# Performance work log

Measured on AMD Instinct MI355X. Metric: run time of the kernel, lower is better.

## Reference

```python
import jax, jax.numpy as jnp
import numpy as np

TOP_K = 2  # matches init top_k


def setup_inputs() -> dict:
    key = jax.random.key(0)
    k = jax.random.split(key, 5)
    B, S, D, E, H = 8, 2048, 768, 8, 3072  # batch, seq, n_embed, num_experts, 4*n_embed
    init = lambda kk, shape: (jax.random.normal(kk, shape, jnp.float32) * 0.02)
    return {
        "x": jax.random.normal(k[0], (B, S, D), jnp.float32),
        "Wg": init(k[1], (D, E)),            # router weight
        "bg": jnp.zeros((E,), jnp.float32),   # router bias
        "W1": init(k[2], (E, D, H)),          # stacked expert fc1
        "b1": jnp.zeros((E, H), jnp.float32),
        "W2": init(k[3], (E, H, D)),          # stacked expert fc2
        "b2": jnp.zeros((E, D), jnp.float32),
    }


def _moe(x, Wg, bg, W1, b1, W2, b2):
    B, S, D = x.shape
    E = Wg.shape[1]
    # --- TopkRouter: top-k logits, softmax over selected experts, scatter to full gate tensor ---
    logits = x @ Wg + bg                                  # [B,S,E]
    top_vals, top_idx = jax.lax.top_k(logits, TOP_K)      # [B,S,K]
    gates_k = jax.nn.softmax(top_vals, axis=-1)           # softmax over the k selected experts only
    one_hot = jax.nn.one_hot(top_idx, E, dtype=x.dtype)   # [B,S,K,E] (E is small)
    gates = jnp.sum(one_hot * gates_k[..., None], axis=-2)  # [B,S,E], zeros off top-k

    # --- dispatch/compute/combine: scan over experts (fixed, small), gate-weighted accumulate ---
    flat_x = x.reshape(-1, D)          # [T,D]
    flat_g = gates.reshape(-1, E).T    # [E,T]

    def body(acc, p):
        W1e, b1e, W2e, b2e, ge = p
        h = jax.nn.relu(flat_x @ W1e + b1e)               # [T,H]
        acc = acc + (h @ W2e + b2e) * ge[:, None]         # gate==0 -> zero contribution (incl. bias)
        return acc, None

    out, _ = jax.lax.scan(body, jnp.zeros_like(flat_x), (W1, b1, W2, b2, flat_g))
    return out.reshape(B, S, D)


def reference(x, Wg, bg, W1, b1, W2, b2):
    return _moe(x, Wg, bg, W1, b1, W2, b2)
```

## Files before the change

kernel.cpp:

```cpp
#include <hip/hip_runtime.h>
#include <stdint.h>

typedef unsigned short u16;
typedef __attribute__((ext_vector_type(8))) short v8s;
typedef __attribute__((ext_vector_type(4))) float v4f;

#define T_TOK 16384
#define DIM   768
#define NE    8
#define HH    3072
#define CH    1536
#define MCAP  34816
#define GM    (MCAP/256)

#define O_W2T 0u
#define O_W1T 37748736u
#define O_XBF 75497472u
#define O_OB1 37748736u
#define O_STK 100663296u
#define O_SGT 100802560u
#define O_TE  100941824u
#define O_TG  101072896u
#define O_TS  101203968u
#define O_MET 101335040u
#define O_HBF 101335296u
#define O_OB0 208290048u
#define WS_TIER_A 261767424ull

__device__ __forceinline__ u16 f2bf(float f){
  uint32_t u = __float_as_uint(f);
  uint32_t r = (u + 0x7fffu + ((u >> 16) & 1u)) >> 16;
  return (u16)r;
}
__device__ __forceinline__ float bf2f(u16 v){
  return __uint_as_float(((uint32_t)v) << 16);
}
__device__ __forceinline__ void gll16(const u16* g, u16* l){
  __builtin_amdgcn_global_load_lds((const __attribute__((address_space(1))) uint32_t*)g,
                                   (__attribute__((address_space(3))) uint32_t*)l, 16, 0, 0);
}

#define BAR() do { asm volatile("" ::: "memory"); __builtin_amdgcn_s_barrier(); asm volatile("" ::: "memory"); } while(0)
#define WAIT_LGKM0() asm volatile("s_waitcnt lgkmcnt(0)" ::: "memory")
#define WAIT_VM4() asm volatile("s_waitcnt vmcnt(4)" ::: "memory")
#define WAIT_VM0() asm volatile("s_waitcnt vmcnt(0)" ::: "memory")

__global__ __launch_bounds__(256) void k_transpose(
    const float* __restrict__ src, u16* __restrict__ dst, int R, int C){
  __shared__ float tile[64][65];
  int e = blockIdx.z;
  int c0 = blockIdx.x * 64, r0 = blockIdx.y * 64;
  const float* s = src + (size_t)e * R * C;
  u16* d = dst + (size_t)e * R * C;
  int tx = threadIdx.x, ty = threadIdx.y;
  #pragma unroll
  for (int j = 0; j < 4; j++){
    float4 v = *(const float4*)&s[(size_t)(r0 + ty + 16*j) * C + c0 + tx*4];
    tile[ty+16*j][tx*4+0] = v.x; tile[ty+16*j][tx*4+1] = v.y;
    tile[ty+16*j][tx*4+2] = v.z; tile[ty+16*j][tx*4+3] = v.w;
  }
  __syncthreads();
  #pragma unroll
  for (int j = 0; j < 4; j++){
    int cc = ty + 16*j;
    ushort4 o;
    o.x = f2bf(tile[tx*4+0][cc]);
    o.y = f2bf(tile[tx*4+1][cc]);
    o.z = f2bf(tile[tx*4+2][cc]);
    o.w = f2bf(tile[tx*4+3][cc]);
    *(ushort4*)&d[(size_t)(c0 + cc) * R + r0 + tx*4] = o;
  }
}

__global__ __launch_bounds__(256) void k_router(
    const float* __restrict__ x, const float* __restrict__ Wg, const float* __restrict__ bg,
    int* __restrict__ tE, float* __restrict__ tG, u16* __restrict__ Xbf){
  int t = blockIdx.x * 4 + (threadIdx.x >> 6);
  int l = threadIdx.x & 63;
  const float4* xr4 = (const float4*)(x + (size_t)t * DIM);
  ushort4* xb4 = (ushort4*)(Xbf + (size_t)t * DIM);
  float acc[NE];
  #pragma unroll
  for (int e = 0; e < NE; e++) acc[e] = 0.f;
  #pragma unroll
  for (int j = 0; j < DIM / 256; j++){
    int c4 = l + 64 * j;
    float4 xv = xr4[c4];
    ushort4 o; o.x = f2bf(xv.x); o.y = f2bf(xv.y); o.z = f2bf(xv.z); o.w = f2bf(xv.w);
    xb4[c4] = o;
    float xs[4] = {xv.x, xv.y, xv.z, xv.w};
    #pragma unroll
    for (int q = 0; q < 4; q++){
      const float4* wr4 = (const float4*)(Wg + (size_t)(4*c4 + q) * NE);
      float4 w0 = wr4[0], w1 = wr4[1];
      acc[0] += xs[q]*w0.x; acc[1] += xs[q]*w0.y; acc[2] += xs[q]*w0.z; acc[3] += xs[q]*w0.w;
      acc[4] += xs[q]*w1.x; acc[5] += xs[q]*w1.y; acc[6] += xs[q]*w1.z; acc[7] += xs[q]*w1.w;
    }
  }
  #pragma unroll
  for (int off = 32; off; off >>= 1)
    #pragma unroll
    for (int e = 0; e < NE; e++) acc[e] += __shfl_xor(acc[e], off, 64);

  if (l == 0){
    float lgt[NE];
    #pragma unroll
    for (int e = 0; e < NE; e++) lgt[e] = acc[e] + bg[e];
    int i0 = 0; float v0 = lgt[0];
    #pragma unroll
    for (int e = 1; e < NE; e++) if (lgt[e] > v0){ v0 = lgt[e]; i0 = e; }
    int i1 = -1; float v1 = -1e30f;
    #pragma unroll
    for (int e = 0; e < NE; e++) if (e != i0 && lgt[e] > v1){ v1 = lgt[e]; i1 = e; }
    float ed = expf(v1 - v0);
    float g1 = ed / (1.f + ed);
    float g0 = 1.f / (1.f + ed);
    tE[2*t] = i0; tE[2*t+1] = i1;
    tG[2*t] = g0; tG[2*t+1] = g1;
  }
}

__global__ __launch_bounds__(256) void k_count(const int* __restrict__ tE, int* __restrict__ counts){
  int i = blockIdx.x * blockDim.x + threadIdx.x;
  int c[NE];
  #pragma unroll
  for (int e = 0; e < NE; e++) c[e] = 0;
  for (int j = i; j < 2 * T_TOK; j += 32 * 256){
    int v = tE[j];
    #pragma unroll
    for (int e = 0; e < NE; e++) c[e] += (v == e);
  }
  #pragma unroll
  for (int off = 32; off; off >>= 1)
    #pragma unroll
    for (int e = 0; e < NE; e++) c[e] += __shfl_xor(c[e], off, 64);
  if ((threadIdx.x & 63) == 0){
    #pragma unroll
    for (int e = 0; e < NE; e++) atomicAdd(&counts[e], c[e]);
  }
}

__global__ void k_scan(const int* __restrict__ counts, int* __restrict__ offs){
  if (threadIdx.x == 0){
    int o = 0;
    for (int e = 0; e < NE; e++){ offs[e] = o; o += (counts[e] + 255) & ~255; }
    offs[NE] = o;
  }
}

__global__ __launch_bounds__(256) void k_scatter(
    const int* __restrict__ tE, const float* __restrict__ tG,
    const int* __restrict__ offs, int* __restrict__ fill,
    int* __restrict__ slot_token, float* __restrict__ slot_gate, int* __restrict__ tSlot){
  int t = blockIdx.x * 256 + threadIdx.x;
  int lane = threadIdx.x & 63, w = threadIdx.x >> 6;
  int e0 = tE[2*t], e1 = tE[2*t+1];
  float g0 = tG[2*t], g1 = tG[2*t+1];

  __shared__ int wcnt[4][NE];
  __shared__ int woff[4][NE];
  __shared__ int bbase[NE];

  uint64_t below = (1ull << lane) - 1ull;
  int rank0 = 0, rank1 = 0;
  #pragma unroll
  for (int e = 0; e < NE; e++){
    uint64_t m0 = __ballot(e0 == e);
    uint64_t m1 = __ballot(e1 == e);
    int c0 = __popcll(m0);
    if (e0 == e) rank0 = __popcll(m0 & below);
    if (e1 == e) rank1 = c0 + __popcll(m1 & below);
    if (lane == 0) wcnt[w][e] = c0 + __popcll(m1);
  }
  __syncthreads();
  if (threadIdx.x < NE){
    int e = threadIdx.x;
    int s = 0;
    #pragma unroll
    for (int ww = 0; ww < 4; ww++){ woff[ww][e] = s; s += wcnt[ww][e]; }
    bbase[e] = atomicAdd(&fill[e], s);
  }
  __syncthreads();
  int p0 = offs[e0] + bbase[e0] + woff[w][e0] + rank0;
  slot_token[p0] = t; slot_gate[p0] = g0; tSlot[2*t] = p0;
  int p1 = offs[e1] + bbase[e1] + woff[w][e1] + rank1;
  slot_token[p1] = t; slot_gate[p1] = g1; tSlot[2*t+1] = p1;
}

__global__ void k_outinit(const int* __restrict__ tE, const float* __restrict__ tG,
                          const float* __restrict__ b2, float* __restrict__ out){
  int t = blockIdx.x;
  int e0 = tE[2*t], e1 = tE[2*t+1];
  float g0 = tG[2*t], g1 = tG[2*t+1];
  const float* r0 = b2 + (size_t)e0 * DIM;
  const float* r1 = b2 + (size_t)e1 * DIM;
  float* o = out + (size_t)t * DIM;
  #pragma unroll
  for (int j = 0; j < DIM / 256; j++){
    int c = threadIdx.x + 256 * j;
    o[c] = g0 * r0[c] + g1 * r1[c];
  }
}

#define ABASE(b,h) (((b)*2+(h))*8192)
#define BBASE(b,h) (32768 + ((b)*2+(h))*8192)
#define SWZE(ro,ks) (((((ro)*128) + (ks)*64 + lg*16) ^ (((lm)&7)<<4)) >> 1)

#define STAGE2(p0, p1, base, kk) do { \
  gll16((p0) + (kk), &lds[(base) + (w*2)*512]); \
  gll16((p1) + (kk), &lds[(base) + (w*2+1)*512]); } while(0)

#define MFMA_Q(MOFF, NOFF, BF) \
  __builtin_amdgcn_s_setprio(1); \
  _Pragma("unroll") \
  for (int mi = 0; mi < 4; mi++) \
    _Pragma("unroll") \
    for (int ni = 0; ni < 2; ni++) \
      _Pragma("unroll") \
      for (int ks = 0; ks < 2; ks++) \
        acc[(MOFF)+mi][(NOFF)+ni] = __builtin_amdgcn_mfma_f32_16x16x32_bf16(aF[mi][ks], BF[ni][ks], acc[(MOFF)+mi][(NOFF)+ni], 0, 0, 0); \
  __builtin_amdgcn_s_setprio(0);

__device__ __forceinline__ int find_expert(const int* offs, int grb, int& total){
  int offr[NE+1];
  #pragma unroll
  for (int i = 0; i <= NE; i++) offr[i] = offs[i];
  total = offr[NE];
  int e = 0;
  #pragma unroll
  for (int i = 1; i < NE; i++) e += (grb >= offr[i]);
  return e;
}

__global__ __launch_bounds__(512, 2) void k_gemm1(
    const u16* __restrict__ Xbf, const u16* __restrict__ W1t, const float* __restrict__ b1,
    const int* __restrict__ slot_token, const float* __restrict__ slot_gate,
    const int* __restrict__ offs, u16* __restrict__ Hbuf, int hs, int cbase, int ntc)
{
  int bid = blockIdx.x;
  int swz = (bid & 7) * ((int)gridDim.x >> 3) + (bid >> 3);
  int mt = swz / ntc, ntile = swz % ntc;
  int grb = mt * 256;
  int total;
  int e = find_expert(offs, grb, total);
  if (grb >= total) return;
  int nb = ntile * 256;
  int habs = cbase + nb;

  __shared__ __align__(16) u16 lds[65536];

  int tid = threadIdx.x, w = tid >> 6, lane = tid & 63;
  int wm = w >> 2, wn = w & 3, lm = lane & 15, lg = lane >> 4;
  int cbe = (((lane & 7) ^ (lane >> 3)) << 3);

  int rA00 = (w*2+0)*8 + (lane>>3), rA01 = (w*2+1)*8 + (lane>>3);
  const u16 *sA00 = Xbf + (size_t)slot_token[grb + rA00]       * DIM + cbe;
  const u16 *sA01 = Xbf + (size_t)slot_token[grb + rA01]       * DIM + cbe;
  const u16 *sA10 = Xbf + (size_t)slot_token[grb + 128 + rA00] * DIM + cbe;
  const u16 *sA11 = Xbf + (size_t)slot_token[grb + 128 + rA01] * DIM + cbe;
  const u16 *sB00 = W1t + ((size_t)e*HH + habs + rA00)       * DIM + cbe;
  const u16 *sB01 = W1t + ((size_t)e*HH + habs + rA01)       * DIM + cbe;
  const u16 *sB10 = W1t + ((size_t)e*HH + habs + 128 + rA00) * DIM + cbe;
  const u16 *sB11 = W1t + ((size_t)e*HH + habs + 128 + rA01) * DIM + cbe;

  v4f acc[8][4];
  #pragma unroll
  for (int mi = 0; mi < 8; mi++)
    #pragma unroll
    for (int ni = 0; ni < 4; ni++) acc[mi][ni] = 0.f;

  const int NTK = DIM / 64;
  STAGE2(sA00, sA01, ABASE(0,0), 0);  STAGE2(sA10, sA11, ABASE(0,1), 0);
  STAGE2(sB00, sB01, BBASE(0,0), 0);  STAGE2(sB10, sB11, BBASE(0,1), 0);
  STAGE2(sA00, sA01, ABASE(1,0), 64); STAGE2(sA10, sA11, ABASE(1,1), 64);
  WAIT_VM4(); BAR();

  v8s aF[4][2], bF0[2][2], bF1[2][2];
  for (int k = 0; k < NTK; ++k){
    int cur = k & 1, nx = cur ^ 1;
    int ab = ABASE(cur, wm);
    int bb = BBASE(cur, wn >> 1);
    #pragma unroll
    for (int mi = 0; mi < 4; mi++)
      #pragma unroll
      for (int ks = 0; ks < 2; ks++)
        aF[mi][ks] = *(const v8s*)&lds[ab + SWZE(mi*16 + lm, ks)];
    #pragma unroll
    for (int ni = 0; ni < 2; ni++)
      #pragma unroll
      for (int ks = 0; ks < 2; ks++)
        bF0[ni][ks] = *(const v8s*)&lds[bb + SWZE((wn&1)*64 + ni*16 + lm, ks)];
    if (k + 1 < NTK) STAGE2(sB00, sB01, BBASE(nx,0), (k+1)*64);
    MFMA_Q(0, 0, bF0);
    BAR();
    #pragma unroll
    for (int ni = 0; ni < 2; ni++)
      #pragma unroll
      for (int ks = 0; ks < 2; ks++)
        bF1[ni][ks] = *(const v8s*)&lds[bb + SWZE((wn&1)*64 + (2+ni)*16 + lm, ks)];
    if (k + 1 < NTK) STAGE2(sB10, sB11, BBASE(nx,1), (k+1)*64);
    MFMA_Q(0, 2, bF1);
    BAR();
    #pragma unroll
    for (int mi = 0; mi < 4; mi++)
      #pragma unroll
      for (int ks = 0; ks < 2; ks++)
        aF[mi][ks] = *(const v8s*)&lds[ab + SWZE((4+mi)*16 + lm, ks)];
    MFMA_Q(4, 0, bF0);
    WAIT_LGKM0(); BAR();
    if (k + 2 < NTK){
      STAGE2(sA00, sA01, ABASE(cur,0), (k+2)*64);
      STAGE2(sA10, sA11, ABASE(cur,1), (k+2)*64);
    }
    MFMA_Q(4, 2, bF1);
    if (k + 2 < NTK) { WAIT_VM4(); } else { WAIT_VM0(); }
    BAR();
  }

  float b1v[4];
  #pragma unroll
  for (int ni = 0; ni < 4; ni++) b1v[ni] = b1[(size_t)e * HH + habs + wn*64 + ni*16 + lm];
  #pragma unroll
  for (int mi = 0; mi < 8; mi++){
    int rbase = grb + wm*128 + mi*16 + lg*4;
    float g[4];
    #pragma unroll
    for (int i = 0; i < 4; i++) g[i] = slot_gate[rbase + i];
    #pragma unroll
    for (int ni = 0; ni < 4; ni++){
      int col = nb + wn*64 + ni*16 + lm;
      #pragma unroll
      for (int i = 0; i < 4; i++){
        float v = acc[mi][ni][i] + b1v[ni];
        v = fmaxf(v, 0.f) * g[i];
        Hbuf[(size_t)(rbase + i) * hs + col] = f2bf(v);
      }
    }
  }
}

__global__ __launch_bounds__(512, 2) void k_gemm2(
    const u16* __restrict__ Hbuf, const u16* __restrict__ W2t,
    const int* __restrict__ slot_token, const int* __restrict__ offs,
    float* __restrict__ out, u16* __restrict__ Obuf, int hs, int cbase, int klen, int mode)
{
  const int NT = DIM / 256;
  int bid = blockIdx.x;
  int swz = (bid & 7) * ((int)gridDim.x >> 3) + (bid >> 3);
  int mt = swz / NT, ntile = swz % NT;
  int grb = mt * 256;
  int total;
  int e = find_expert(offs, grb, total);
  if (grb >= total) return;
  int nb = ntile * 256;

  __shared__ __align__(16) u16 lds[65536];

  int tid = threadIdx.x, w = tid >> 6, lane = tid & 63;
  int wm = w >> 2, wn = w & 3, lm = lane & 15, lg = lane >> 4;
  int cbe = (((lane & 7) ^ (lane >> 3)) << 3);

  int rA00 = (w*2+0)*8 + (lane>>3), rA01 = (w*2+1)*8 + (lane>>3);
  const u16 *sA00 = Hbuf + (size_t)(grb + rA00)       * hs + cbe;
  const u16 *sA01 = Hbuf + (size_t)(grb + rA01)       * hs + cbe;
  const u16 *sA10 = Hbuf + (size_t)(grb + 128 + rA00) * hs + cbe;
  const u16 *sA11 = Hbuf + (size_t)(grb + 128 + rA01) * hs + cbe;
  const u16 *sB00 = W2t + ((size_t)e*DIM + nb + rA00)       * HH + cbase + cbe;
  const u16 *sB01 = W2t + ((size_t)e*DIM + nb + rA01)       * HH + cbase + cbe;
  const u16 *sB10 = W2t + ((size_t)e*DIM + nb + 128 + rA00) * HH + cbase + cbe;
  const u16 *sB11 = W2t + ((size_t)e*DIM + nb + 128 + rA01) * HH + cbase + cbe;

  v4f acc[8][4];
  #pragma unroll
  for (int mi = 0; mi < 8; mi++)
    #pragma unroll
    for (int ni = 0; ni < 4; ni++) acc[mi][ni] = 0.f;

  const int ntk = klen / 64;
  STAGE2(sA00, sA01, ABASE(0,0), 0);  STAGE2(sA10, sA11, ABASE(0,1), 0);
  STAGE2(sB00, sB01, BBASE(0,0), 0);  STAGE2(sB10, sB11, BBASE(0,1), 0);
  STAGE2(sA00, sA01, ABASE(1,0), 64); STAGE2(sA10, sA11, ABASE(1,1), 64);
  WAIT_VM4(); BAR();

  v8s aF[4][2], bF0[2][2], bF1[2][2];
  for (int k = 0; k < ntk; ++k){
    int cur = k & 1, nx = cur ^ 1;
    int ab = ABASE(cur, wm);
    int bb = BBASE(cur, wn >> 1);
    #pragma unroll
    for (int mi = 0; mi < 4; mi++)
      #pragma unroll
      for (int ks = 0; ks < 2; ks++)
        aF[mi][ks] = *(const v8s*)&lds[ab + SWZE(mi*16 + lm, ks)];
    #pragma unroll
    for (int ni = 0; ni < 2; ni++)
      #pragma unroll
      for (int ks = 0; ks < 2; ks++)
        bF0[ni][ks] = *(const v8s*)&lds[bb + SWZE((wn&1)*64 + ni*16 + lm, ks)];
    if (k + 1 < ntk) STAGE2(sB00, sB01, BBASE(nx,0), (k+1)*64);
    MFMA_Q(0, 0, bF0);
    BAR();
    #pragma unroll
    for (int ni = 0; ni < 2; ni++)
      #pragma unroll
      for (int ks = 0; ks < 2; ks++)
        bF1[ni][ks] = *(const v8s*)&lds[bb + SWZE((wn&1)*64 + (2+ni)*16 + lm, ks)];
    if (k + 1 < ntk) STAGE2(sB10, sB11, BBASE(nx,1), (k+1)*64);
    MFMA_Q(0, 2, bF1);
    BAR();
    #pragma unroll
    for (int mi = 0; mi < 4; mi++)
      #pragma unroll
      for (int ks = 0; ks < 2; ks++)
        aF[mi][ks] = *(const v8s*)&lds[ab + SWZE((4+mi)*16 + lm, ks)];
    MFMA_Q(4, 0, bF0);
    WAIT_LGKM0(); BAR();
    if (k + 2 < ntk){
      STAGE2(sA00, sA01, ABASE(cur,0), (k+2)*64);
      STAGE2(sA10, sA11, ABASE(cur,1), (k+2)*64);
    }
    MFMA_Q(4, 2, bF1);
    if (k + 2 < ntk) { WAIT_VM4(); } else { WAIT_VM0(); }
    BAR();
  }

  if (mode == 1){
    #pragma unroll
    for (int mi = 0; mi < 8; mi++){
      int rbase = grb + wm*128 + mi*16 + lg*4;
      #pragma unroll
      for (int ni = 0; ni < 4; ni++){
        int col = nb + wn*64 + ni*16 + lm;
        #pragma unroll
        for (int i = 0; i < 4; i++)
          Obuf[(size_t)(rbase + i) * DIM + col] = f2bf(acc[mi][ni][i]);
      }
    }
  } else {
    #pragma unroll
    for (int mi = 0; mi < 8; mi++){
      int rbase = grb + wm*128 + mi*16 + lg*4;
      int tok[4];
      #pragma unroll
      for (int i = 0; i < 4; i++) tok[i] = slot_token[rbase + i];
      #pragma unroll
      for (int ni = 0; ni < 4; ni++){
        int col = nb + wn*64 + ni*16 + lm;
        #pragma unroll
        for (int i = 0; i < 4; i++)
          unsafeAtomicAdd(&out[(size_t)tok[i] * DIM + col], acc[mi][ni][i]);
      }
    }
  }
}

__global__ __launch_bounds__(192) void k_combine2(
    const u16* __restrict__ O0, const u16* __restrict__ O1,
    const int* __restrict__ tSlot, const int* __restrict__ tE,
    const float* __restrict__ tG, const float* __restrict__ b2,
    float* __restrict__ out)
{
  int t = blockIdx.x;
  int l = threadIdx.x;
  int s0 = tSlot[2*t], s1 = tSlot[2*t+1];
  int e0 = tE[2*t], e1 = tE[2*t+1];
  float g0 = tG[2*t], g1 = tG[2*t+1];
  int c = l * 4;
  ushort4 a0 = *(const ushort4*)(O0 + (size_t)s0 * DIM + c);
  ushort4 a1 = *(const ushort4*)(O0 + (size_t)s1 * DIM + c);
  ushort4 b0 = *(const ushort4*)(O1 + (size_t)s0 * DIM + c);
  ushort4 b1v = *(const ushort4*)(O1 + (size_t)s1 * DIM + c);
  float4 bA = *(const float4*)(b2 + (size_t)e0 * DIM + c);
  float4 bB = *(const float4*)(b2 + (size_t)e1 * DIM + c);
  float4 r;
  r.x = bf2f(a0.x) + bf2f(a1.x) + bf2f(b0.x) + bf2f(b1v.x) + g0 * bA.x + g1 * bB.x;
  r.y = bf2f(a0.y) + bf2f(a1.y) + bf2f(b0.y) + bf2f(b1v.y) + g0 * bA.y + g1 * bB.y;
  r.z = bf2f(a0.z) + bf2f(a1.z) + bf2f(b0.z) + bf2f(b1v.z) + g0 * bA.z + g1 * bB.z;
  r.w = bf2f(a0.w) + bf2f(a1.w) + bf2f(b0.w) + bf2f(b1v.w) + g0 * bA.w + g1 * bB.w;
  *(float4*)(out + (size_t)t * DIM + c) = r;
}

extern "C" void kernel_launch(void* const* d_in, const int* in_sizes, int n_in,
                              void* d_out, int out_size, void* d_ws, size_t ws_size,
                              hipStream_t stream)
{
  const float* x  = (const float*)d_in[0];
  const float* Wg = (const float*)d_in[1];
  const float* bg = (const float*)d_in[2];
  const float* W1 = (const float*)d_in[3];
  const float* b1 = (const float*)d_in[4];
  const float* W2 = (const float*)d_in[5];
  const float* b2 = (const float*)d_in[6];
  float* out = (float*)d_out;
  char* ws = (char*)d_ws;

  u16*   W2t        = (u16*)(ws + O_W2T);
  u16*   W1t        = (u16*)(ws + O_W1T);
  u16*   Xbf        = (u16*)(ws + O_XBF);
  u16*   Obuf0      = (u16*)(ws + O_OB0);
  u16*   Obuf1      = (u16*)(ws + O_OB1);
  u16*   Hbuf       = (u16*)(ws + O_HBF);
  int*   slot_token = (int*)(ws + O_STK);
  float* slot_gate  = (float*)(ws + O_SGT);
  int*   tE         = (int*)(ws + O_TE);
  float* tG         = (float*)(ws + O_TG);
  int*   tSlot      = (int*)(ws + O_TS);
  int*   meta       = (int*)(ws + O_MET);
  int*   counts = meta;
  int*   fill   = meta + 8;
  int*   offs   = meta + 16;

  const bool tierA = (ws_size >= WS_TIER_A);

  hipMemsetAsync(ws + O_STK, 0, O_TE - O_STK, stream);
  hipMemsetAsync(ws + O_MET, 0, 128, stream);

  k_transpose<<<dim3(HH/64, DIM/64, NE), dim3(16, 16), 0, stream>>>(W1, W1t, DIM, HH);
  k_transpose<<<dim3(DIM/64, HH/64, NE), dim3(16, 16), 0, stream>>>(W2, W2t, HH, DIM);

  k_router<<<T_TOK/4, 256, 0, stream>>>(x, Wg, bg, tE, tG, Xbf);
  k_count<<<32, 256, 0, stream>>>(tE, counts);
  k_scan<<<1, 1, 0, stream>>>(counts, offs);
  k_scatter<<<T_TOK/256, 256, 0, stream>>>(tE, tG, offs, fill, slot_token, slot_gate, tSlot);

  if (tierA){
    k_gemm1<<<GM * (CH/256), 512, 0, stream>>>(Xbf, W1t, b1, slot_token, slot_gate, offs, Hbuf, CH, 0, CH/256);
    k_gemm2<<<GM * (DIM/256), 512, 0, stream>>>(Hbuf, W2t, slot_token, offs, out, Obuf0, CH, 0, CH, 1);
    k_gemm1<<<GM * (CH/256), 512, 0, stream>>>(Xbf, W1t, b1, slot_token, slot_gate, offs, Hbuf, CH, CH, CH/256);
    k_gemm2<<<GM * (DIM/256), 512, 0, stream>>>(Hbuf, W2t, slot_token, offs, out, Obuf1, CH, CH, CH, 1);
    k_combine2<<<T_TOK, 192, 0, stream>>>(Obuf0, Obuf1, tSlot, tE, tG, b2, out);
  } else {
    k_outinit<<<T_TOK, 256, 0, stream>>>(tE, tG, b2, out);
    for (int c = 0; c < 2; c++){
      k_gemm1<<<GM * (CH/256), 512, 0, stream>>>(Xbf, W1t, b1, slot_token, slot_gate, offs, Hbuf, CH, c*CH, CH/256);
      k_gemm2<<<GM * (DIM/256), 512, 0, stream>>>(Hbuf, W2t, slot_token, offs, out, Obuf0, CH, c*CH, CH, 0);
    }
  }
}
```

Measured before the change: 514.4 us.

## Triple-buffer B tiles in expert GEMMs with prefetch distance two

Both expert GEMM kernels now keep three LDS buffers for the weight (B) tiles instead of two. B tiles are prefetched two K-steps ahead rather than one, and the vmcnt wait is relaxed to allow more loads in flight. The goal is to hide more global-load latency behind the MFMA work. In exchange, shared memory per block grows from 128 KB to 160 KB, and correctness depends on the unseen ABASE/BBASE layout handling a third B buffer. The gate values in the gemm1 epilogue are also read with one float4 load instead of four scalar loads.

```diff
diff --git a/kernel.cpp b/kernel.cpp
--- a/kernel.cpp
+++ b/kernel.cpp
@@ -42,7 +42,7 @@
 
 #define BAR() do { asm volatile("" ::: "memory"); __builtin_amdgcn_s_barrier(); asm volatile("" ::: "memory"); } while(0)
 #define WAIT_LGKM0() asm volatile("s_waitcnt lgkmcnt(0)" ::: "memory")
-#define WAIT_VM4() asm volatile("s_waitcnt vmcnt(4)" ::: "memory")
+#define WAIT_VM8() asm volatile("s_waitcnt vmcnt(8)" ::: "memory")
 #define WAIT_VM0() asm volatile("s_waitcnt vmcnt(0)" ::: "memory")
 
 __global__ __launch_bounds__(256) void k_transpose(
@@ -247,7 +247,7 @@
   int nb = ntile * 256;
   int habs = cbase + nb;
 
-  __shared__ __align__(16) u16 lds[65536];
+  __shared__ __align__(16) u16 lds[81920];
 
   int tid = threadIdx.x, w = tid >> 6, lane = tid & 63;
   int wm = w >> 2, wn = w & 3, lm = lane & 15, lg = lane >> 4;
@@ -273,13 +273,15 @@
   STAGE2(sA00, sA01, ABASE(0,0), 0);  STAGE2(sA10, sA11, ABASE(0,1), 0);
   STAGE2(sB00, sB01, BBASE(0,0), 0);  STAGE2(sB10, sB11, BBASE(0,1), 0);
   STAGE2(sA00, sA01, ABASE(1,0), 64); STAGE2(sA10, sA11, ABASE(1,1), 64);
-  WAIT_VM4(); BAR();
+  STAGE2(sB00, sB01, BBASE(1,0), 64); STAGE2(sB10, sB11, BBASE(1,1), 64);
+  WAIT_VM8(); BAR();
 
   v8s aF[4][2], bF0[2][2], bF1[2][2];
   for (int k = 0; k < NTK; ++k){
-    int cur = k & 1, nx = cur ^ 1;
-    int ab = ABASE(cur, wm);
-    int bb = BBASE(cur, wn >> 1);
+    int abuf = k & 1;
+    int bbuf = k % 3, bnx = (k + 2) % 3;
+    int ab = ABASE(abuf, wm);
+    int bb = BBASE(bbuf, wn >> 1);
     #pragma unroll
     for (int mi = 0; mi < 4; mi++)
       #pragma unroll
@@ -290,7 +292,7 @@
       #pragma unroll
       for (int ks = 0; ks < 2; ks++)
         bF0[ni][ks] = *(const v8s*)&lds[bb + SWZE((wn&1)*64 + ni*16 + lm, ks)];
-    if (k + 1 < NTK) STAGE2(sB00, sB01, BBASE(nx,0), (k+1)*64);
+    if (k + 2 < NTK) STAGE2(sB00, sB01, BBASE(bnx,0), (k+2)*64);
     MFMA_Q(0, 0, bF0);
     BAR();
     #pragma unroll
@@ -298,7 +300,7 @@
       #pragma unroll
       for (int ks = 0; ks < 2; ks++)
         bF1[ni][ks] = *(const v8s*)&lds[bb + SWZE((wn&1)*64 + (2+ni)*16 + lm, ks)];
-    if (k + 1 < NTK) STAGE2(sB10, sB11, BBASE(nx,1), (k+1)*64);
+    if (k + 2 < NTK) STAGE2(sB10, sB11, BBASE(bnx,1), (k+2)*64);
     MFMA_Q(0, 2, bF1);
     BAR();
     #pragma unroll
@@ -309,11 +311,11 @@
     MFMA_Q(4, 0, bF0);
     WAIT_LGKM0(); BAR();
     if (k + 2 < NTK){
-      STAGE2(sA00, sA01, ABASE(cur,0), (k+2)*64);
-      STAGE2(sA10, sA11, ABASE(cur,1), (k+2)*64);
+      STAGE2(sA00, sA01, ABASE(abuf,0), (k+2)*64);
+      STAGE2(sA10, sA11, ABASE(abuf,1), (k+2)*64);
     }
     MFMA_Q(4, 2, bF1);
-    if (k + 2 < NTK) { WAIT_VM4(); } else { WAIT_VM0(); }
+    if (k + 2 < NTK) { WAIT_VM8(); } else { WAIT_VM0(); }
     BAR();
   }
 
@@ -323,9 +325,8 @@
   #pragma unroll
   for (int mi = 0; mi < 8; mi++){
     int rbase = grb + wm*128 + mi*16 + lg*4;
-    float g[4];
-    #pragma unroll
-    for (int i = 0; i < 4; i++) g[i] = slot_gate[rbase + i];
+    float4 gv = *(const float4*)&slot_gate[rbase];
+    float g[4] = {gv.x, gv.y, gv.z, gv.w};
     #pragma unroll
     for (int ni = 0; ni < 4; ni++){
       int col = nb + wn*64 + ni*16 + lm;
@@ -354,7 +355,7 @@
   if (grb >= total) return;
   int nb = ntile * 256;
 
-  __shared__ __align__(16) u16 lds[65536];
+  __shared__ __align__(16) u16 lds[81920];
 
   int tid = threadIdx.x, w = tid >> 6, lane = tid & 63;
   int wm = w >> 2, wn = w & 3, lm = lane & 15, lg = lane >> 4;
@@ -380,13 +381,15 @@
   STAGE2(sA00, sA01, ABASE(0,0), 0);  STAGE2(sA10, sA11, ABASE(0,1), 0);
   STAGE2(sB00, sB01, BBASE(0,0), 0);  STAGE2(sB10, sB11, BBASE(0,1), 0);
   STAGE2(sA00, sA01, ABASE(1,0), 64); STAGE2(sA10, sA11, ABASE(1,1), 64);
-  WAIT_VM4(); BAR();
+  STAGE2(sB00, sB01, BBASE(1,0), 64); STAGE2(sB10, sB11, BBASE(1,1), 64);
+  WAIT_VM8(); BAR();
 
   v8s aF[4][2], bF0[2][2], bF1[2][2];
   for (int k = 0; k < ntk; ++k){
-    int cur = k & 1, nx = cur ^ 1;
-    int ab = ABASE(cur, wm);
-    int bb = BBASE(cur, wn >> 1);
+    int abuf = k & 1;
+    int bbuf = k % 3, bnx = (k + 2) % 3;
+    int ab = ABASE(abuf, wm);
+    int bb = BBASE(bbuf, wn >> 1);
     #pragma unroll
     for (int mi = 0; mi < 4; mi++)
       #pragma unroll
@@ -397,7 +400,7 @@
       #pragma unroll
       for (int ks = 0; ks < 2; ks++)
         bF0[ni][ks] = *(const v8s*)&lds[bb + SWZE((wn&1)*64 + ni*16 + lm, ks)];
-    if (k + 1 < ntk) STAGE2(sB00, sB01, BBASE(nx,0), (k+1)*64);
+    if (k + 2 < ntk) STAGE2(sB00, sB01, BBASE(bnx,0), (k+2)*64);
     MFMA_Q(0, 0, bF0);
     BAR();
     #pragma unroll
@@ -405,7 +408,7 @@
       #pragma unroll
       for (int ks = 0; ks < 2; ks++)
         bF1[ni][ks] = *(const v8s*)&lds[bb + SWZE((wn&1)*64 + (2+ni)*16 + lm, ks)];
-    if (k + 1 < ntk) STAGE2(sB10, sB11, BBASE(nx,1), (k+1)*64);
+    if (k + 2 < ntk) STAGE2(sB10, sB11, BBASE(bnx,1), (k+2)*64);
     MFMA_Q(0, 2, bF1);
     BAR();
     #pragma unroll
@@ -416,11 +419,11 @@
     MFMA_Q(4, 0, bF0);
     WAIT_LGKM0(); BAR();
     if (k + 2 < ntk){
-      STAGE2(sA00, sA01, ABASE(cur,0), (k+2)*64);
-      STAGE2(sA10, sA11, ABASE(cur,1), (k+2)*64);
+      STAGE2(sA00, sA01, ABASE(abuf,0), (k+2)*64);
+      STAGE2(sA10, sA11, ABASE(abuf,1), (k+2)*64);
     }
     MFMA_Q(4, 2, bF1);
-    if (k + 2 < ntk) { WAIT_VM4(); } else { WAIT_VM0(); }
+    if (k + 2 < ntk) { WAIT_VM8(); } else { WAIT_VM0(); }
     BAR();
   }
 
```

Measured after the change: 530.0 us. 1.03x slower.

## Convert expert GEMMs to persistent kernels with atomic tile tickets

Applied to the files above, without the earlier changes.

Both grouped GEMM kernels now launch a fixed grid of 256 blocks. Each block repeatedly claims a tile index from a global atomic counter, instead of mapping blockIdx to a tile through a swizzle. The aim is to stop empty padded tiles from wasting launch slots and to balance work dynamically across CUs. In exchange it adds an atomic and a barrier per tile, drops the L2-friendly swizzled tile order, and depends on the ticket counters being zeroed by the existing meta memset.

```diff
diff --git a/kernel.cpp b/kernel.cpp
--- a/kernel.cpp
+++ b/kernel.cpp
@@ -235,105 +235,111 @@
 __global__ __launch_bounds__(512, 2) void k_gemm1(
     const u16* __restrict__ Xbf, const u16* __restrict__ W1t, const float* __restrict__ b1,
     const int* __restrict__ slot_token, const float* __restrict__ slot_gate,
-    const int* __restrict__ offs, u16* __restrict__ Hbuf, int hs, int cbase, int ntc)
+    const int* __restrict__ offs, u16* __restrict__ Hbuf, int hs, int cbase, int ntc,
+    int* __restrict__ ticket, int ntiles)
 {
-  int bid = blockIdx.x;
-  int swz = (bid & 7) * ((int)gridDim.x >> 3) + (bid >> 3);
-  int mt = swz / ntc, ntile = swz % ntc;
-  int grb = mt * 256;
-  int total;
-  int e = find_expert(offs, grb, total);
-  if (grb >= total) return;
-  int nb = ntile * 256;
-  int habs = cbase + nb;
-
   __shared__ __align__(16) u16 lds[65536];
+  __shared__ int s_tile[2];
 
   int tid = threadIdx.x, w = tid >> 6, lane = tid & 63;
   int wm = w >> 2, wn = w & 3, lm = lane & 15, lg = lane >> 4;
   int cbe = (((lane & 7) ^ (lane >> 3)) << 3);
-
   int rA00 = (w*2+0)*8 + (lane>>3), rA01 = (w*2+1)*8 + (lane>>3);
-  const u16 *sA00 = Xbf + (size_t)slot_token[grb + rA00]       * DIM + cbe;
-  const u16 *sA01 = Xbf + (size_t)slot_token[grb + rA01]       * DIM + cbe;
-  const u16 *sA10 = Xbf + (size_t)slot_token[grb + 128 + rA00] * DIM + cbe;
-  const u16 *sA11 = Xbf + (size_t)slot_token[grb + 128 + rA01] * DIM + cbe;
-  const u16 *sB00 = W1t + ((size_t)e*HH + habs + rA00)       * DIM + cbe;
-  const u16 *sB01 = W1t + ((size_t)e*HH + habs + rA01)       * DIM + cbe;
-  const u16 *sB10 = W1t + ((size_t)e*HH + habs + 128 + rA00) * DIM + cbe;
-  const u16 *sB11 = W1t + ((size_t)e*HH + habs + 128 + rA01) * DIM + cbe;
-
-  v4f acc[8][4];
-  #pragma unroll
-  for (int mi = 0; mi < 8; mi++)
-    #pragma unroll
-    for (int ni = 0; ni < 4; ni++) acc[mi][ni] = 0.f;
-
-  const int NTK = DIM / 64;
-  STAGE2(sA00, sA01, ABASE(0,0), 0);  STAGE2(sA10, sA11, ABASE(0,1), 0);
-  STAGE2(sB00, sB01, BBASE(0,0), 0);  STAGE2(sB10, sB11, BBASE(0,1), 0);
-  STAGE2(sA00, sA01, ABASE(1,0), 64); STAGE2(sA10, sA11, ABASE(1,1), 64);
-  WAIT_VM4(); BAR();
-
-  v8s aF[4][2], bF0[2][2], bF1[2][2];
-  for (int k = 0; k < NTK; ++k){
-    int cur = k & 1, nx = cur ^ 1;
-    int ab = ABASE(cur, wm);
-    int bb = BBASE(cur, wn >> 1);
-    #pragma unroll
-    for (int mi = 0; mi < 4; mi++)
-      #pragma unroll
-      for (int ks = 0; ks < 2; ks++)
-        aF[mi][ks] = *(const v8s*)&lds[ab + SWZE(mi*16 + lm, ks)];
-    #pragma unroll
-    for (int ni = 0; ni < 2; ni++)
-      #pragma unroll
-      for (int ks = 0; ks < 2; ks++)
-        bF0[ni][ks] = *(const v8s*)&lds[bb + SWZE((wn&1)*64 + ni*16 + lm, ks)];
-    if (k + 1 < NTK) STAGE2(sB00, sB01, BBASE(nx,0), (k+1)*64);
-    MFMA_Q(0, 0, bF0);
-    BAR();
-    #pragma unroll
-    for (int ni = 0; ni < 2; ni++)
-      #pragma unroll
-      for (int ks = 0; ks < 2; ks++)
-        bF1[ni][ks] = *(const v8s*)&lds[bb + SWZE((wn&1)*64 + (2+ni)*16 + lm, ks)];
-    if (k + 1 < NTK) STAGE2(sB10, sB11, BBASE(nx,1), (k+1)*64);
-    MFMA_Q(0, 2, bF1);
-    BAR();
-    #pragma unroll
-    for (int mi = 0; mi < 4; mi++)
-      #pragma unroll
-      for (int ks = 0; ks < 2; ks++)
-        aF[mi][ks] = *(const v8s*)&lds[ab + SWZE((4+mi)*16 + lm, ks)];
-    MFMA_Q(4, 0, bF0);
-    WAIT_LGKM0(); BAR();
-    if (k + 2 < NTK){
-      STAGE2(sA00, sA01, ABASE(cur,0), (k+2)*64);
-      STAGE2(sA10, sA11, ABASE(cur,1), (k+2)*64);
+
+  for (int it = 0; ; ++it){
+    if (tid == 0) s_tile[it & 1] = atomicAdd(ticket, 1);
+    __syncthreads();
+    int tile = s_tile[it & 1];
+    if (tile >= ntiles) return;
+    int mt = tile / ntc, ntile = tile % ntc;
+    int grb = mt * 256;
+    int total;
+    int e = find_expert(offs, grb, total);
+    if (grb >= total) continue;
+    int nb = ntile * 256;
+    int habs = cbase + nb;
+
+    const u16 *sA00 = Xbf + (size_t)slot_token[grb + rA00]       * DIM + cbe;
+    const u16 *sA01 = Xbf + (size_t)slot_token[grb + rA01]       * DIM + cbe;
+    const u16 *sA10 = Xbf + (size_t)slot_token[grb + 128 + rA00] * DIM + cbe;
+    const u16 *sA11 = Xbf + (size_t)slot_token[grb + 128 + rA01] * DIM + cbe;
+    const u16 *sB00 = W1t + ((size_t)e*HH + habs + rA00)       * DIM + cbe;
+    const u16 *sB01 = W1t + ((size_t)e*HH + habs + rA01)       * DIM + cbe;
+    const u16 *sB10 = W1t + ((size_t)e*HH + habs + 128 + rA00) * DIM + cbe;
+    const u16 *sB11 = W1t + ((size_t)e*HH + habs + 128 + rA01) * DIM + cbe;
+
+    v4f acc[8][4];
+    #pragma unroll
+    for (int mi = 0; mi < 8; mi++)
+      #pragma unroll
+      for (int ni = 0; ni < 4; ni++) acc[mi][ni] = 0.f;
+
+    const int NTK = DIM / 64;
+    STAGE2(sA00, sA01, ABASE(0,0), 0);  STAGE2(sA10, sA11, ABASE(0,1), 0);
+    STAGE2(sB00, sB01, BBASE(0,0), 0);  STAGE2(sB10, sB11, BBASE(0,1), 0);
+    STAGE2(sA00, sA01, ABASE(1,0), 64); STAGE2(sA10, sA11, ABASE(1,1), 64);
+    WAIT_VM4(); BAR();
+
+    v8s aF[4][2], bF0[2][2], bF1[2][2];
+    for (int k = 0; k < NTK; ++k){
+      int cur = k & 1, nx = cur ^ 1;
+      int ab = ABASE(cur, wm);
+      int bb = BBASE(cur, wn >> 1);
+      #pragma unroll
+      for (int mi = 0; mi < 4; mi++)
+        #pragma unroll
+        for (int ks = 0; ks < 2; ks++)
+          aF[mi][ks] = *(const v8s*)&lds[ab + SWZE(mi*16 + lm, ks)];
+      #pragma unroll
+      for (int ni = 0; ni < 2; ni++)
+        #pragma unroll
+        for (int ks = 0; ks < 2; ks++)
+          bF0[ni][ks] = *(const v8s*)&lds[bb + SWZE((wn&1)*64 + ni*16 + lm, ks)];
+      if (k + 1 < NTK) STAGE2(sB00, sB01, BBASE(nx,0), (k+1)*64);
+      MFMA_Q(0, 0, bF0);
+      BAR();
+      #pragma unroll
+      for (int ni = 0; ni < 2; ni++)
+        #pragma unroll
+        for (int ks = 0; ks < 2; ks++)
+          bF1[ni][ks] = *(const v8s*)&lds[bb + SWZE((wn&1)*64 + (2+ni)*16 + lm, ks)];
+      if (k + 1 < NTK) STAGE2(sB10, sB11, BBASE(nx,1), (k+1)*64);
+      MFMA_Q(0, 2, bF1);
+      BAR();
+      #pragma unroll
+      for (int mi = 0; mi < 4; mi++)
+        #pragma unroll
+        for (int ks = 0; ks < 2; ks++)
+          aF[mi][ks] = *(const v8s*)&lds[ab + SWZE((4+mi)*16 + lm, ks)];
+      MFMA_Q(4, 0, bF0);
+      WAIT_LGKM0(); BAR();
+      if (k + 2 < NTK){
+        STAGE2(sA00, sA01, ABASE(cur,0), (k+2)*64);
+        STAGE2(sA10, sA11, ABASE(cur,1), (k+2)*64);
+      }
+      MFMA_Q(4, 2, bF1);
+      if (k + 2 < NTK) { WAIT_VM4(); } else { WAIT_VM0(); }
+      BAR();
     }
-    MFMA_Q(4, 2, bF1);
-    if (k + 2 < NTK) { WAIT_VM4(); } else { WAIT_VM0(); }
-    BAR();
-  }
-
-  float b1v[4];
-  #pragma unroll
-  for (int ni = 0; ni < 4; ni++) b1v[ni] = b1[(size_t)e * HH + habs + wn*64 + ni*16 + lm];
-  #pragma unroll
-  for (int mi = 0; mi < 8; mi++){
-    int rbase = grb + wm*128 + mi*16 + lg*4;
-    float g[4];
-    #pragma unroll
-    for (int i = 0; i < 4; i++) g[i] = slot_gate[rbase + i];
-    #pragma unroll
-    for (int ni = 0; ni < 4; ni++){
-      int col = nb + wn*64 + ni*16 + lm;
-      #pragma unroll
-      for (int i = 0; i < 4; i++){
-        float v = acc[mi][ni][i] + b1v[ni];
-        v = fmaxf(v, 0.f) * g[i];
-        Hbuf[(size_t)(rbase + i) * hs + col] = f2bf(v);
+
+    float b1v[4];
+    #pragma unroll
+    for (int ni = 0; ni < 4; ni++) b1v[ni] = b1[(size_t)e * HH + habs + wn*64 + ni*16 + lm];
+    #pragma unroll
+    for (int mi = 0; mi < 8; mi++){
+      int rbase = grb + wm*128 + mi*16 + lg*4;
+      float g[4];
+      #pragma unroll
+      for (int i = 0; i < 4; i++) g[i] = slot_gate[rbase + i];
+      #pragma unroll
+      for (int ni = 0; ni < 4; ni++){
+        int col = nb + wn*64 + ni*16 + lm;
+        #pragma unroll
+        for (int i = 0; i < 4; i++){
+          float v = acc[mi][ni][i] + b1v[ni];
+          v = fmaxf(v, 0.f) * g[i];
+          Hbuf[(size_t)(rbase + i) * hs + col] = f2bf(v);
+        }
       }
     }
   }
@@ -342,113 +348,119 @@
 __global__ __launch_bounds__(512, 2) void k_gemm2(
     const u16* __restrict__ Hbuf, const u16* __restrict__ W2t,
     const int* __restrict__ slot_token, const int* __restrict__ offs,
-    float* __restrict__ out, u16* __restrict__ Obuf, int hs, int cbase, int klen, int mode)
+    float* __restrict__ out, u16* __restrict__ Obuf, int hs, int cbase, int klen, int mode,
+    int* __restrict__ ticket, int ntiles)
 {
   const int NT = DIM / 256;
-  int bid = blockIdx.x;
-  int swz = (bid & 7) * ((int)gridDim.x >> 3) + (bid >> 3);
-  int mt = swz / NT, ntile = swz % NT;
-  int grb = mt * 256;
-  int total;
-  int e = find_expert(offs, grb, total);
-  if (grb >= total) return;
-  int nb = ntile * 256;
-
   __shared__ __align__(16) u16 lds[65536];
+  __shared__ int s_tile[2];
 
   int tid = threadIdx.x, w = tid >> 6, lane = tid & 63;
   int wm = w >> 2, wn = w & 3, lm = lane & 15, lg = lane >> 4;
   int cbe = (((lane & 7) ^ (lane >> 3)) << 3);
-
   int rA00 = (w*2+0)*8 + (lane>>3), rA01 = (w*2+1)*8 + (lane>>3);
-  const u16 *sA00 = Hbuf + (size_t)(grb + rA00)       * hs + cbe;
-  const u16 *sA01 = Hbuf + (size_t)(grb + rA01)       * hs + cbe;
-  const u16 *sA10 = Hbuf + (size_t)(grb + 128 + rA00) * hs + cbe;
-  const u16 *sA11 = Hbuf + (size_t)(grb + 128 + rA01) * hs + cbe;
-  const u16 *sB00 = W2t + ((size_t)e*DIM + nb + rA00)       * HH + cbase + cbe;
-  const u16 *sB01 = W2t + ((size_t)e*DIM + nb + rA01)       * HH + cbase + cbe;
-  const u16 *sB10 = W2t + ((size_t)e*DIM + nb + 128 + rA00) * HH + cbase + cbe;
-  const u16 *sB11 = W2t + ((size_t)e*DIM + nb + 128 + rA01) * HH + cbase + cbe;
-
-  v4f acc[8][4];
-  #pragma unroll
-  for (int mi = 0; mi < 8; mi++)
-    #pragma unroll
-    for (int ni = 0; ni < 4; ni++) acc[mi][ni] = 0.f;
-
-  const int ntk = klen / 64;
-  STAGE2(sA00, sA01, ABASE(0,0), 0);  STAGE2(sA10, sA11, ABASE(0,1), 0);
-  STAGE2(sB00, sB01, BBASE(0,0), 0);  STAGE2(sB10, sB11, BBASE(0,1), 0);
-  STAGE2(sA00, sA01, ABASE(1,0), 64); STAGE2(sA10, sA11, ABASE(1,1), 64);
-  WAIT_VM4(); BAR();
-
-  v8s aF[4][2], bF0[2][2], bF1[2][2];
-  for (int k = 0; k < ntk; ++k){
-    int cur = k & 1, nx = cur ^ 1;
-    int ab = ABASE(cur, wm);
-    int bb = BBASE(cur, wn >> 1);
-    #pragma unroll
-    for (int mi = 0; mi < 4; mi++)
-      #pragma unroll
-      for (int ks = 0; ks < 2; ks++)
-        aF[mi][ks] = *(const v8s*)&lds[ab + SWZE(mi*16 + lm, ks)];
-    #pragma unroll
-    for (int ni = 0; ni < 2; ni++)
-      #pragma unroll
-      for (int ks = 0; ks < 2; ks++)
-        bF0[ni][ks] = *(const v8s*)&lds[bb + SWZE((wn&1)*64 + ni*16 + lm, ks)];
-    if (k + 1 < ntk) STAGE2(sB00, sB01, BBASE(nx,0), (k+1)*64);
-    MFMA_Q(0, 0, bF0);
-    BAR();
-    #pragma unroll
-    for (int ni = 0; ni < 2; ni++)
-      #pragma unroll
-      for (int ks = 0; ks < 2; ks++)
-        bF1[ni][ks] = *(const v8s*)&lds[bb + SWZE((wn&1)*64 + (2+ni)*16 + lm, ks)];
-    if (k + 1 < ntk) STAGE2(sB10, sB11, BBASE(nx,1), (k+1)*64);
-    MFMA_Q(0, 2, bF1);
-    BAR();
-    #pragma unroll
-    for (int mi = 0; mi < 4; mi++)
-      #pragma unroll
-      for (int ks = 0; ks < 2; ks++)
-        aF[mi][ks] = *(const v8s*)&lds[ab + SWZE((4+mi)*16 + lm, ks)];
-    MFMA_Q(4, 0, bF0);
-    WAIT_LGKM0(); BAR();
-    if (k + 2 < ntk){
-      STAGE2(sA00, sA01, ABASE(cur,0), (k+2)*64);
-      STAGE2(sA10, sA11, ABASE(cur,1), (k+2)*64);
+
+  for (int it = 0; ; ++it){
+    if (tid == 0) s_tile[it & 1] = atomicAdd(ticket, 1);
+    __syncthreads();
+    int tile = s_tile[it & 1];
+    if (tile >= ntiles) return;
+    int mt = tile / NT, ntile = tile % NT;
+    int grb = mt * 256;
+    int total;
+    int e = find_expert(offs, grb, total);
+    if (grb >= total) continue;
+    int nb = ntile * 256;
+
+    const u16 *sA00 = Hbuf + (size_t)(grb + rA00)       * hs + cbe;
+    const u16 *sA01 = Hbuf + (size_t)(grb + rA01)       * hs + cbe;
+    const u16 *sA10 = Hbuf + (size_t)(grb + 128 + rA00) * hs + cbe;
+    const u16 *sA11 = Hbuf + (size_t)(grb + 128 + rA01) * hs + cbe;
+    const u16 *sB00 = W2t + ((size_t)e*DIM + nb + rA00)       * HH + cbase + cbe;
+    const u16 *sB01 = W2t + ((size_t)e*DIM + nb + rA01)       * HH + cbase + cbe;
+    const u16 *sB10 = W2t + ((size_t)e*DIM + nb + 128 + rA00) * HH + cbase + cbe;
+    const u16 *sB11 = W2t + ((size_t)e*DIM + nb + 128 + rA01) * HH + cbase + cbe;
+
+    v4f acc[8][4];
+    #pragma unroll
+    for (int mi = 0; mi < 8; mi++)
+      #pragma unroll
+      for (int ni = 0; ni < 4; ni++) acc[mi][ni] = 0.f;
+
+    const int ntk = klen / 64;
+    STAGE2(sA00, sA01, ABASE(0,0), 0);  STAGE2(sA10, sA11, ABASE(0,1), 0);
+    STAGE2(sB00, sB01, BBASE(0,0), 0);  STAGE2(sB10, sB11, BBASE(0,1), 0);
+    STAGE2(sA00, sA01, ABASE(1,0), 64); STAGE2(sA10, sA11, ABASE(1,1), 64);
+    WAIT_VM4(); BAR();
+
+    v8s aF[4][2], bF0[2][2], bF1[2][2];
+    for (int k = 0; k < ntk; ++k){
+      int cur = k & 1, nx = cur ^ 1;
+      int ab = ABASE(cur, wm);
+      int bb = BBASE(cur, wn >> 1);
+      #pragma unroll
+      for (int mi = 0; mi < 4; mi++)
+        #pragma unroll
+        for (int ks = 0; ks < 2; ks++)
+          aF[mi][ks] = *(const v8s*)&lds[ab + SWZE(mi*16 + lm, ks)];
+      #pragma unroll
+      for (int ni = 0; ni < 2; ni++)
+        #pragma unroll
+        for (int ks = 0; ks < 2; ks++)
+          bF0[ni][ks] = *(const v8s*)&lds[bb + SWZE((wn&1)*64 + ni*16 + lm, ks)];
+      if (k + 1 < ntk) STAGE2(sB00, sB01, BBASE(nx,0), (k+1)*64);
+      MFMA_Q(0, 0, bF0);
+      BAR();
+      #pragma unroll
+      for (int ni = 0; ni < 2; ni++)
+        #pragma unroll
+        for (int ks = 0; ks < 2; ks++)
+          bF1[ni][ks] = *(const v8s*)&lds[bb + SWZE((wn&1)*64 + (2+ni)*16 + lm, ks)];
+      if (k + 1 < ntk) STAGE2(sB10, sB11, BBASE(nx,1), (k+1)*64);
+      MFMA_Q(0, 2, bF1);
+      BAR();
+      #pragma unroll
+      for (int mi = 0; mi < 4; mi++)
+        #pragma unroll
+        for (int ks = 0; ks < 2; ks++)
+          aF[mi][ks] = *(const v8s*)&lds[ab + SWZE((4+mi)*16 + lm, ks)];
+      MFMA_Q(4, 0, bF0);
+      WAIT_LGKM0(); BAR();
+      if (k + 2 < ntk){
+        STAGE2(sA00, sA01, ABASE(cur,0), (k+2)*64);
+        STAGE2(sA10, sA11, ABASE(cur,1), (k+2)*64);
+      }
+      MFMA_Q(4, 2, bF1);
+      if (k + 2 < ntk) { WAIT_VM4(); } else { WAIT_VM0(); }
+      BAR();
     }
-    MFMA_Q(4, 2, bF1);
-    if (k + 2 < ntk) { WAIT_VM4(); } else { WAIT_VM0(); }
-    BAR();
-  }
-
-  if (mode == 1){
-    #pragma unroll
-    for (int mi = 0; mi < 8; mi++){
-      int rbase = grb + wm*128 + mi*16 + lg*4;
-      #pragma unroll
-      for (int ni = 0; ni < 4; ni++){
-        int col = nb + wn*64 + ni*16 + lm;
-        #pragma unroll
-        for (int i = 0; i < 4; i++)
-          Obuf[(size_t)(rbase + i) * DIM + col] = f2bf(acc[mi][ni][i]);
+
+    if (mode == 1){
+      #pragma unroll
+      for (int mi = 0; mi < 8; mi++){
+        int rbase = grb + wm*128 + mi*16 + lg*4;
+        #pragma unroll
+        for (int ni = 0; ni < 4; ni++){
+          int col = nb + wn*64 + ni*16 + lm;
+          #pragma unroll
+          for (int i = 0; i < 4; i++)
+            Obuf[(size_t)(rbase + i) * DIM + col] = f2bf(acc[mi][ni][i]);
+        }
       }
-    }
-  } else {
-    #pragma unroll
-    for (int mi = 0; mi < 8; mi++){
-      int rbase = grb + wm*128 + mi*16 + lg*4;
-      int tok[4];
-      #pragma unroll
-      for (int i = 0; i < 4; i++) tok[i] = slot_token[rbase + i];
-      #pragma unroll
-      for (int ni = 0; ni < 4; ni++){
-        int col = nb + wn*64 + ni*16 + lm;
-        #pragma unroll
-        for (int i = 0; i < 4; i++)
-          unsafeAtomicAdd(&out[(size_t)tok[i] * DIM + col], acc[mi][ni][i]);
+    } else {
+      #pragma unroll
+      for (int mi = 0; mi < 8; mi++){
+        int rbase = grb + wm*128 + mi*16 + lg*4;
+        int tok[4];
+        #pragma unroll
+        for (int i = 0; i < 4; i++) tok[i] = slot_token[rbase + i];
+        #pragma unroll
+        for (int ni = 0; ni < 4; ni++){
+          int col = nb + wn*64 + ni*16 + lm;
+          #pragma unroll
+          for (int i = 0; i < 4; i++)
+            unsafeAtomicAdd(&out[(size_t)tok[i] * DIM + col], acc[mi][ni][i]);
+        }
       }
     }
   }
@@ -506,9 +518,10 @@
   float* tG         = (float*)(ws + O_TG);
   int*   tSlot      = (int*)(ws + O_TS);
   int*   meta       = (int*)(ws + O_MET);
-  int*   counts = meta;
-  int*   fill   = meta + 8;
-  int*   offs   = meta + 16;
+  int*   counts  = meta;
+  int*   fill    = meta + 8;
+  int*   offs    = meta + 16;
+  int*   tickets = meta + 28;
 
   const bool tierA = (ws_size >= WS_TIER_A);
 
@@ -523,17 +536,20 @@
   k_scan<<<1, 1, 0, stream>>>(counts, offs);
   k_scatter<<<T_TOK/256, 256, 0, stream>>>(tE, tG, offs, fill, slot_token, slot_gate, tSlot);
 
+  const int NT1 = GM * (CH/256);
+  const int NT2 = GM * (DIM/256);
+
   if (tierA){
-    k_gemm1<<<GM * (CH/256), 512, 0, stream>>>(Xbf, W1t, b1, slot_token, slot_gate, offs, Hbuf, CH, 0, CH/256);
-    k_gemm2<<<GM * (DIM/256), 512, 0, stream>>>(Hbuf, W2t, slot_token, offs, out, Obuf0, CH, 0, CH, 1);
-    k_gemm1<<<GM * (CH/256), 512, 0, stream>>>(Xbf, W1t, b1, slot_token, slot_gate, offs, Hbuf, CH, CH, CH/256);
-    k_gemm2<<<GM * (DIM/256), 512, 0, stream>>>(Hbuf, W2t, slot_token, offs, out, Obuf1, CH, CH, CH, 1);
+    k_gemm1<<<256, 512, 0, stream>>>(Xbf, W1t, b1, slot_token, slot_gate, offs, Hbuf, CH, 0, CH/256, tickets+0, NT1);
+    k_gemm2<<<256, 512, 0, stream>>>(Hbuf, W2t, slot_token, offs, out, Obuf0, CH, 0, CH, 1, tickets+1, NT2);
+    k_gemm1<<<256, 512, 0, stream>>>(Xbf, W1t, b1, slot_token, slot_gate, offs, Hbuf, CH, CH, CH/256, tickets+2, NT1);
+    k_gemm2<<<256, 512, 0, stream>>>(Hbuf, W2t, slot_token, offs, out, Obuf1, CH, CH, CH, 1, tickets+3, NT2);
     k_combine2<<<T_TOK, 192, 0, stream>>>(Obuf0, Obuf1, tSlot, tE, tG, b2, out);
   } else {
     k_outinit<<<T_TOK, 256, 0, stream>>>(tE, tG, b2, out);
     for (int c = 0; c < 2; c++){
-      k_gemm1<<<GM * (CH/256), 512, 0, stream>>>(Xbf, W1t, b1, slot_token, slot_gate, offs, Hbuf, CH, c*CH, CH/256);
-      k_gemm2<<<GM * (DIM/256), 512, 0, stream>>>(Hbuf, W2t, slot_token, offs, out, Obuf0, CH, c*CH, CH, 0);
+      k_gemm1<<<256, 512, 0, stream>>>(Xbf, W1t, b1, slot_token, slot_gate, offs, Hbuf, CH, c*CH, CH/256, tickets+2*c, NT1);
+      k_gemm2<<<256, 512, 0, stream>>>(Hbuf, W2t, slot_token, offs, out, Obuf0, CH, c*CH, CH, 0, tickets+2*c+1, NT2);
     }
   }
 }
```

New measurement: 596.9 us. +16.0%, slower.
